# Performance work log

Hardware: AMD Instinct MI355X
Metric: run time of the kernel (lower is better)

The kernel has to match this reference:

```python
import jax, jax.numpy as jnp
import numpy as np

BS, N = 8, 2000
ALPHA = 0.2  # LeakyReLU slope
NEG = -9e15


def _gat_head(x, adj, W, a):
    # x: [bs,N,Fin], W: [Fin,Fout], a: [2*Fout]
    h = x @ W                                   # [bs,N,F]
    F_ = W.shape[-1]
    # e_ij = lrelu(h_i . a[:F] + h_j . a[F:])  (decomposed form of concat+matmul)
    src = h @ a[:F_]                            # [bs,N]
    dst = h @ a[F_:]                            # [bs,N]
    e = jax.nn.leaky_relu(src[:, :, None] + dst[:, None, :], ALPHA)  # [bs,N,N]
    att = jnp.where(adj[None] > 0, e, NEG)
    att = jax.nn.softmax(att, axis=-1)
    return jax.nn.elu(att @ h)                  # [bs,N,F]


def _gat_multihead(x, adj, W, a):
    # W: [H,Fin,Fout], a: [H,2*Fout] -> concat heads on feature dim
    out = jax.vmap(_gat_head, in_axes=(None, None, 0, 0))(x, adj, W, a)  # [H,bs,N,F]
    H, bs, n, F_ = out.shape
    return jnp.moveaxis(out, 0, 2).reshape(bs, n, H * F_)


def setup_inputs() -> dict:
    key = jax.random.key(0)
    ks = jax.random.split(key, 20)
    g = 1.414

    def xavu(k, shape, gain=1.0):
        fan_in, fan_out = shape[-2], shape[-1]
        lim = gain * np.sqrt(6.0 / (fan_in + fan_out))
        return jax.random.uniform(k, shape, jnp.float32, -lim, lim)

    x = jax.random.normal(ks[0], (BS, N, 1), jnp.float32)
    adj = jax.random.randint(ks[1], (N, N), 0, 2).astype(jnp.float32)
    inp = {
        "x": x, "adj": adj,
        "W1": xavu(ks[2], (4, 1, 8), g), "a1": xavu(ks[3], (4, 16, 1), g)[..., 0],
        "W2": xavu(ks[4], (3, 32, 16), g), "a2": xavu(ks[5], (3, 32, 1), g)[..., 0],
        "pw1": xavu(ks[6], (32, 1))[:, 0], "pb1": jnp.zeros((1,), jnp.float32),
        "pw2": xavu(ks[7], (48, 1))[:, 0], "pb2": jnp.zeros((1,), jnp.float32),
        "fc1_w": xavu(ks[8], (3 * N, 600)), "fc1_b": jnp.zeros((600,), jnp.float32),
        "fc2_w": xavu(ks[9], (600, 256)), "fc2_b": jnp.zeros((256,), jnp.float32),
        "fc3_w": xavu(ks[10], (256, 64)), "fc3_b": jnp.zeros((64,), jnp.float32),
        "fc4_w": xavu(ks[11], (64, 32)), "fc4_b": jnp.zeros((32,), jnp.float32),
        "fc5_w": xavu(ks[12], (32, 2)), "fc5_b": jnp.zeros((2,), jnp.float32),
    }
    return inp


def reference(x, adj, W1, a1, W2, a2, pw1, pb1, pw2, pb2,
              fc1_w, fc1_b, fc2_w, fc2_b, fc3_w, fc3_b, fc4_w, fc4_b, fc5_w, fc5_b):
    # dropout layers are identity in eval mode
    x0 = jnp.mean(x, axis=-1)                       # [bs,N]
    h = _gat_multihead(x, adj, W1, a1)              # [bs,N,32]
    x1 = h @ pw1 + pb1                              # [bs,N]
    h = _gat_multihead(h, adj, W2, a2)              # [bs,N,48]
    x2 = h @ pw2 + pb2                              # [bs,N]
    z = jnp.concatenate([x0, x1, x2], axis=1)       # [bs,3N]
    z = jax.nn.elu(z @ fc1_w + fc1_b)
    z = jax.nn.elu(z @ fc2_w + fc2_b)
    z1 = jax.nn.elu(z @ fc3_w + fc3_b)              # output [bs,64]
    z = jax.nn.elu(z1 @ fc4_w + fc4_b)
    gat_out = z @ fc5_w + fc5_b                     # [bs,2]
    return (z1, gat_out)
```

## Files before the change

kernel.cpp:

```cpp
#include <hip/hip_runtime.h>
#include <hip/hip_bf16.h>
#include <cmath>

#define N_NODES 2000
#define BS 8

typedef __attribute__((ext_vector_type(8))) short short8v;
typedef __attribute__((ext_vector_type(4))) float float4v;

__device__ __forceinline__ float elu_f(float v) { return v > 0.f ? v : expm1f(v); }

__device__ __forceinline__ unsigned short f32_bf16u(float f) {
    __hip_bfloat16 h = __float2bfloat16(f);
    unsigned short u;
    __builtin_memcpy(&u, &h, 2);
    return u;
}
__device__ __forceinline__ short f32_bf16(float f) { return (short)f32_bf16u(f); }

__device__ __forceinline__ unsigned cvt_pk_bf16(float a, float b) {
    unsigned r;
    asm("v_cvt_pk_bf16_f32 %0, %1, %2" : "=v"(r) : "v"(a), "v"(b));
    return r;
}

__global__ __launch_bounds__(256) void pack_kernel(
    const float* __restrict__ adj,
    unsigned* __restrict__ maskT32,
    short* __restrict__ hT) {
    int bx = blockIdx.x;
    int tid = threadIdx.x;
    if (bx < N_NODES) {
        int row = bx;
        int lane = tid & 63, wv = tid >> 6;
        for (int wq = wv; wq < 32; wq += 4) {
            int j = wq * 64 + lane;
            bool on = (j < N_NODES) && (adj[(size_t)row * N_NODES + j] > 0.f);
            unsigned long long bal = __ballot(on);
            if (lane == 0) {
                maskT32[(size_t)(2 * wq) * 2048 + row] = (unsigned)bal;
                maskT32[(size_t)(2 * wq + 1) * 2048 + row] = (unsigned)(bal >> 32);
            }
        }
        return;
    }
    for (int i = tid; i < 24 * 16 * 48; i += 256) {
        int bh = i / 768, rem = i % 768, f = rem / 48, n = N_NODES + rem % 48;
        hT[((size_t)bh * 16 + f) * 2048 + n] = 0;
    }
}

__global__ __launch_bounds__(256) void att1_kernel(
    const unsigned* __restrict__ maskT32,
    const float* __restrict__ x,
    const float* __restrict__ W1, const float* __restrict__ a1,
    float* __restrict__ o1) {
    __shared__ float2 sPQ[2048];
    __shared__ short sXb[2048];
    __shared__ float2 redmm[256];
    int tid = threadIdx.x;
    int head = blockIdx.y, b = blockIdx.z;

    float ws = 0.f, wd = 0.f;
    #pragma unroll
    for (int f = 0; f < 8; ++f) {
        float wv = W1[head * 8 + f];
        ws = fmaf(wv, a1[head * 16 + f], ws);
        wd = fmaf(wv, a1[head * 16 + 8 + f], wd);
    }

    float mn = 1e30f, mx = -1e30f;
    for (int n = tid; n < 2048; n += 256) {
        float xv = (n < N_NODES) ? x[(size_t)b * N_NODES + n] : 0.f;
        sXb[n] = f32_bf16(xv);
        if (n < N_NODES) { mn = fminf(mn, xv); mx = fmaxf(mx, xv); }
    }
    redmm[tid] = make_float2(mn, mx);
    __syncthreads();
    for (int s = 128; s > 0; s >>= 1) {
        if (tid < s) {
            redmm[tid].x = fminf(redmm[tid].x, redmm[tid + s].x);
            redmm[tid].y = fmaxf(redmm[tid].y, redmm[tid + s].y);
        }
        __syncthreads();
    }
    float md = wd >= 0.f ? wd * redmm[0].y : wd * redmm[0].x;

    for (int n = tid; n < 2048; n += 256) {
        if (n < N_NODES) {
            float d = wd * x[(size_t)b * N_NODES + n] - md;
            sPQ[n] = make_float2(__expf(d), __expf(0.2f * d));
        } else {
            sPQ[n] = make_float2(0.f, 0.f);
        }
    }
    __syncthreads();

    int lane = tid & 63;
    int wave = __builtin_amdgcn_readfirstlane(tid >> 6);
    int t = blockIdx.x * 4 + wave;
    if (t >= 125) return;
    int rs = lane & 15;
    int g = lane >> 4;
    int row = t * 16 + rs;

    float xr = x[(size_t)b * N_NODES + row];
    float u = ws * xr + md;
    float c = __expf(-0.8f * u);

    unsigned fill = (rs == 1) ? 0x3F803F80u : 0u;
    bool isx = (rs == 0);

    float4v acc = {0.f, 0.f, 0.f, 0.f};

    for (int jc = 0; jc < 64; ++jc) {
        int jb = jc * 32 + g * 8;
        float w[8];
        #pragma unroll
        for (int e2 = 0; e2 < 4; ++e2) {
            float4 pq2 = *(const float4*)(&sPQ[jb + e2 * 2]);
            w[e2 * 2 + 0] = fmaxf(pq2.x, c * pq2.y);
            w[e2 * 2 + 1] = fmaxf(pq2.z, c * pq2.w);
        }
        unsigned mby = maskT32[(size_t)jc * 2048 + row] >> (g * 8);
        #pragma unroll
        for (int e = 0; e < 8; ++e)
            w[e] = (mby & (1u << e)) ? w[e] : 0.f;
        uint4 au;
        au.x = cvt_pk_bf16(w[0], w[1]);
        au.y = cvt_pk_bf16(w[2], w[3]);
        au.z = cvt_pk_bf16(w[4], w[5]);
        au.w = cvt_pk_bf16(w[6], w[7]);
        short8v av;
        __builtin_memcpy(&av, &au, 16);
        uint4 xv4 = *(const uint4*)(sXb + jb);
        uint4 bu;
        bu.x = isx ? xv4.x : fill;
        bu.y = isx ? xv4.y : fill;
        bu.z = isx ? xv4.z : fill;
        bu.w = isx ? xv4.w : fill;
        short8v bv;
        __builtin_memcpy(&bv, &bu, 16);
        acc = __builtin_amdgcn_mfma_f32_16x16x32_bf16(av, bv, acc, 0, 0, 0);
    }

    #pragma unroll
    for (int reg = 0; reg < 4; ++reg) {
        int crow = g * 4 + reg;
        float nm = __shfl(acc[reg], lane & 48, 64);
        float dn = __shfl(acc[reg], (lane & 48) | 1, 64);
        float ratio = dn > 0.f ? nm / dn : 0.f;
        if (rs < 8) {
            float v = ratio * W1[head * 8 + rs];
            v = v > 0.f ? v : expm1f(v);
            o1[((size_t)(b * N_NODES + t * 16 + crow)) * 32 + head * 8 + rs] = v;
        }
    }
}

__global__ __launch_bounds__(256) void prep2_kernel(
    const float* __restrict__ o1, const float* __restrict__ W2,
    const float* __restrict__ a2,
    short* __restrict__ hT, float* __restrict__ s2, float* __restrict__ d2) {
    __shared__ float sW[1536];
    int tid = threadIdx.x;
    for (int i = tid; i < 1536; i += 256) sW[i] = W2[i];
    __syncthreads();
    int idx = blockIdx.x * 256 + tid;
    if (idx >= BS * 3 * N_NODES) return;
    int b = idx / 6000, r = idx % 6000, h = r / N_NODES, n = r % N_NODES;
    int bh = b * 3 + h;
    float in[32];
    const float4* ip = (const float4*)(o1 + ((size_t)b * N_NODES + n) * 32);
    #pragma unroll
    for (int q = 0; q < 8; ++q) {
        float4 v = ip[q];
        in[4 * q] = v.x; in[4 * q + 1] = v.y; in[4 * q + 2] = v.z; in[4 * q + 3] = v.w;
    }
    float hv[16];
    #pragma unroll
    for (int f = 0; f < 16; ++f) hv[f] = 0.f;
    #pragma unroll
    for (int k = 0; k < 32; ++k) {
        float ik = in[k];
        #pragma unroll
        for (int f = 0; f < 16; ++f) hv[f] = fmaf(ik, sW[h * 512 + k * 16 + f], hv[f]);
    }
    float sr = 0.f, ds = 0.f;
    #pragma unroll
    for (int f = 0; f < 16; ++f) {
        hT[((size_t)bh * 16 + f) * 2048 + n] = f32_bf16(hv[f]);
        sr = fmaf(hv[f], a2[h * 32 + f], sr);
        ds = fmaf(hv[f], a2[h * 32 + 16 + f], ds);
    }
    s2[(size_t)bh * N_NODES + n] = sr;
    d2[(size_t)bh * N_NODES + n] = ds;
}

__global__ __launch_bounds__(256) void att2_kernel(
    const unsigned* __restrict__ maskT32,
    const short* __restrict__ hT,
    const float* __restrict__ s2, const float* __restrict__ d2,
    float* __restrict__ o2) {
    __shared__ float2 sPQ[2048];
    __shared__ float red[256];
    int tid = threadIdx.x;
    int head = blockIdx.y, b = blockIdx.z, bh = b * 3 + head;
    const float* dp = d2 + (size_t)bh * N_NODES;

    float mx = -1e30f;
    for (int n = tid; n < N_NODES; n += 256) mx = fmaxf(mx, dp[n]);
    red[tid] = mx;
    __syncthreads();
    for (int s = 128; s > 0; s >>= 1) {
        if (tid < s) red[tid] = fmaxf(red[tid], red[tid + s]);
        __syncthreads();
    }
    float md = red[0];
    for (int n = tid; n < 2048; n += 256) {
        if (n < N_NODES) {
            float d = dp[n] - md;
            sPQ[n] = make_float2(__expf(d), __expf(0.2f * d));
        } else {
            sPQ[n] = make_float2(0.f, 0.f);
        }
    }
    __syncthreads();

    int lane = tid & 63;
    int wave = __builtin_amdgcn_readfirstlane(tid >> 6);
    int t = blockIdx.x * 4 + wave;
    if (t >= 125) return;
    int rs = lane & 15;
    int g = lane >> 4;
    int row = t * 16 + rs;

    float sv = s2[(size_t)bh * N_NODES + row];
    float u = sv + md;
    float c = __expf(-0.8f * u);
    const short* hb = hT + ((size_t)bh * 16 + rs) * 2048;

    const unsigned one2 = 0x3F803F80u;
    uint4 ou = make_uint4(one2, one2, one2, one2);
    short8v onesv;
    __builtin_memcpy(&onesv, &ou, 16);

    float4v acc = {0.f, 0.f, 0.f, 0.f};
    float4v accd = {0.f, 0.f, 0.f, 0.f};

    for (int jc = 0; jc < 64; ++jc) {
        int jb = jc * 32 + g * 8;
        float w[8];
        #pragma unroll
        for (int e2 = 0; e2 < 4; ++e2) {
            float4 pq2 = *(const float4*)(&sPQ[jb + e2 * 2]);
            w[e2 * 2 + 0] = fmaxf(pq2.x, c * pq2.y);
            w[e2 * 2 + 1] = fmaxf(pq2.z, c * pq2.w);
        }
        unsigned mby = maskT32[(size_t)jc * 2048 + row] >> (g * 8);
        #pragma unroll
        for (int e = 0; e < 8; ++e)
            w[e] = (mby & (1u << e)) ? w[e] : 0.f;
        uint4 au;
        au.x = cvt_pk_bf16(w[0], w[1]);
        au.y = cvt_pk_bf16(w[2], w[3]);
        au.z = cvt_pk_bf16(w[4], w[5]);
        au.w = cvt_pk_bf16(w[6], w[7]);
        short8v av;
        __builtin_memcpy(&av, &au, 16);
        short8v bv = *(const short8v*)(hb + jb);
        acc = __builtin_amdgcn_mfma_f32_16x16x32_bf16(av, bv, acc, 0, 0, 0);
        accd = __builtin_amdgcn_mfma_f32_16x16x32_bf16(av, onesv, accd, 0, 0, 0);
    }

    #pragma unroll
    for (int reg = 0; reg < 4; ++reg) {
        int crow = g * 4 + reg;
        float dn = accd[reg];
        float v = dn > 0.f ? acc[reg] / dn : 0.f;
        v = v > 0.f ? v : expm1f(v);
        o2[((size_t)(b * N_NODES + t * 16 + crow)) * 48 + head * 16 + rs] = v;
    }
}

__global__ __launch_bounds__(256) void fc1_splitk_kernel(
    const float* __restrict__ x,
    const float* __restrict__ o1, const float* __restrict__ o2,
    const float* __restrict__ pw1, const float* __restrict__ pb1,
    const float* __restrict__ pw2, const float* __restrict__ pb2,
    const float* __restrict__ W, float* __restrict__ partial) {
    const int K = 6000, O = 600, KS = 71;
    __shared__ float sz[BS][KS];
    int tid = threadIdx.x;
    int kt = blockIdx.y;
    int k0 = kt * KS;
    int len = (k0 + KS <= K) ? KS : (K - k0);
    float pb1v = pb1[0], pb2v = pb2[0];
    for (int i = tid; i < BS * len; i += 256) {
        int bb = i / len, k = k0 + i % len;
        float v;
        if (k < 2000) {
            v = x[bb * 2000 + k];
        } else if (k < 4000) {
            const float* op = o1 + ((size_t)bb * 2000 + (k - 2000)) * 32;
            float s = pb1v;
            #pragma unroll
            for (int q = 0; q < 32; ++q) s = fmaf(op[q], pw1[q], s);
            v = s;
        } else {
            const float* op = o2 + ((size_t)bb * 2000 + (k - 4000)) * 48;
            float s = pb2v;
            #pragma unroll
            for (int q = 0; q < 48; ++q) s = fmaf(op[q], pw2[q], s);
            v = s;
        }
        sz[bb][i % len] = v;
    }
    __syncthreads();
    int o = blockIdx.x * 256 + tid;
    float acc[BS] = {0.f, 0.f, 0.f, 0.f, 0.f, 0.f, 0.f, 0.f};
    if (o < O) {
        for (int k = 0; k < len; ++k) {
            float w = W[(size_t)(k0 + k) * O + o];
            #pragma unroll
            for (int b = 0; b < BS; ++b) acc[b] = fmaf(sz[b][k], w, acc[b]);
        }
        #pragma unroll
        for (int b = 0; b < BS; ++b)
            partial[((size_t)kt * BS + b) * O + o] = acc[b];
    }
}

__global__ __launch_bounds__(256) void fc2_splitk_kernel(
    const float* __restrict__ p1, const float* __restrict__ b1,
    const float* __restrict__ W, float* __restrict__ partial) {
    const int K = 600, O = 256, KS = 38;
    __shared__ float sz[BS][KS];
    int tid = threadIdx.x;
    int kt = blockIdx.y;
    int k0 = kt * KS;
    int k1 = k0 + KS < K ? k0 + KS : K;
    int len = k1 - k0;
    for (int i = tid; i < BS * len; i += 256) {
        int bb = i / len, k = k0 + i % len;
        float a = b1[k];
        #pragma unroll 5
        for (int q = 0; q < 85; ++q) a += p1[((size_t)q * BS + bb) * 600 + k];
        sz[bb][i % len] = elu_f(a);
    }
    __syncthreads();
    int o = tid;
    float acc[BS] = {0.f, 0.f, 0.f, 0.f, 0.f, 0.f, 0.f, 0.f};
    for (int k = 0; k < len; ++k) {
        float w = W[(size_t)(k0 + k) * O + o];
        #pragma unroll
        for (int b = 0; b < BS; ++b) acc[b] = fmaf(sz[b][k], w, acc[b]);
    }
    #pragma unroll
    for (int b = 0; b < BS; ++b)
        partial[((size_t)kt * BS + b) * O + o] = acc[b];
}

__global__ __launch_bounds__(256) void fc_tail_kernel(
    const float* __restrict__ p2, const float* __restrict__ b2,
    const float* __restrict__ w3, const float* __restrict__ b3,
    const float* __restrict__ w4, const float* __restrict__ b4,
    const float* __restrict__ w5, const float* __restrict__ b5,
    float* __restrict__ outp) {
    int b = blockIdx.x, tid = threadIdx.x;
    __shared__ float t2[256], red[256], z1[64], z4[32];
    {
        float a = b2[tid];
        #pragma unroll
        for (int kt = 0; kt < 16; ++kt) a += p2[((size_t)kt * BS + b) * 256 + tid];
        t2[tid] = elu_f(a);
    }
    __syncthreads();
    {
        int o = tid & 63, ks = tid >> 6;
        float a = 0.f;
        for (int k = ks; k < 256; k += 4) a = fmaf(t2[k], w3[k * 64 + o], a);
        red[tid] = a;
        __syncthreads();
        if (ks == 0) {
            float v = red[o] + red[64 + o] + red[128 + o] + red[192 + o] + b3[o];
            v = elu_f(v);
            z1[o] = v;
            outp[b * 64 + o] = v;
        }
    }
    __syncthreads();
    if (tid < 32) {
        float v = b4[tid];
        #pragma unroll
        for (int k = 0; k < 64; ++k) v = fmaf(z1[k], w4[k * 32 + tid], v);
        z4[tid] = elu_f(v);
    }
    __syncthreads();
    if (tid < 2) {
        float v = b5[tid];
        #pragma unroll
        for (int k = 0; k < 32; ++k) v = fmaf(z4[k], w5[k * 2 + tid], v);
        outp[BS * 64 + b * 2 + tid] = v;
    }
}

extern "C" void kernel_launch(void* const* d_in, const int* in_sizes, int n_in,
                              void* d_out, int out_size, void* d_ws, size_t ws_size,
                              hipStream_t stream) {
    const float* x    = (const float*)d_in[0];
    const float* adj  = (const float*)d_in[1];
    const float* W1   = (const float*)d_in[2];
    const float* a1   = (const float*)d_in[3];
    const float* W2   = (const float*)d_in[4];
    const float* a2   = (const float*)d_in[5];
    const float* pw1  = (const float*)d_in[6];
    const float* pb1  = (const float*)d_in[7];
    const float* pw2  = (const float*)d_in[8];
    const float* pb2  = (const float*)d_in[9];
    const float* fc1w = (const float*)d_in[10];
    const float* fc1b = (const float*)d_in[11];
    const float* fc2w = (const float*)d_in[12];
    const float* fc2b = (const float*)d_in[13];
    const float* fc3w = (const float*)d_in[14];
    const float* fc3b = (const float*)d_in[15];
    const float* fc4w = (const float*)d_in[16];
    const float* fc4b = (const float*)d_in[17];
    const float* fc5w = (const float*)d_in[18];
    const float* fc5b = (const float*)d_in[19];
    float* outp = (float*)d_out;

    float* ws = (float*)d_ws;
    size_t off = 0;
    auto alloc = [&](size_t n) {
        float* p = ws + off;
        off += (n + 63) & ~(size_t)63;
        return p;
    };
    float* o1 = alloc((size_t)BS * N_NODES * 32);
    float* s2 = alloc((size_t)24 * N_NODES);
    float* d2 = alloc((size_t)24 * N_NODES);
    short* hT = (short*)alloc((size_t)24 * 16 * 2048 / 2);
    float* o2 = alloc((size_t)BS * N_NODES * 48);
    const int KT1 = 85;
    float* p1 = alloc((size_t)KT1 * BS * 600);
    float* p2 = alloc((size_t)16 * BS * 256);
    unsigned* maskT32 = (unsigned*)alloc((size_t)64 * 2048);

    pack_kernel<<<N_NODES + 1, 256, 0, stream>>>(adj, maskT32, hT);
    att1_kernel<<<dim3(32, 4, BS), 256, 0, stream>>>(maskT32, x, W1, a1, o1);
    prep2_kernel<<<(BS * 3 * N_NODES + 255) / 256, 256, 0, stream>>>(o1, W2, a2, hT, s2, d2);
    att2_kernel<<<dim3(32, 3, BS), 256, 0, stream>>>(maskT32, hT, s2, d2, o2);
    fc1_splitk_kernel<<<dim3(3, KT1), 256, 0, stream>>>(
        x, o1, o2, pw1, pb1, pw2, pb2, fc1w, p1);
    fc2_splitk_kernel<<<dim3(1, 16), 256, 0, stream>>>(p1, fc1b, fc2w, p2);
    fc_tail_kernel<<<BS, 256, 0, stream>>>(
        p2, fc2b, fc3w, fc3b, fc4w, fc4b, fc5w, fc5b, outp);
}
```

Baseline: 130.3 us.

## Split attention neighbor dimension in halves with flash-style partial merge kernels

Both attention kernels now split the neighbor (j) dimension into two halves, doubling the grid. Each half computes its own max shift and writes unnormalized numerator and denominator partials, which new finish kernels rescale and merge before applying ELU. The x-to-bf16 conversion moves into pack_kernel, and the block reductions switch to wave shuffles. The aim is more parallelism and a shorter per-block serial loop, at the cost of two extra launches and extra global traffic for the partials.

```diff
diff --git a/kernel.cpp b/kernel.cpp
--- a/kernel.cpp
+++ b/kernel.cpp
@@ -18,16 +18,16 @@
 }
 __device__ __forceinline__ short f32_bf16(float f) { return (short)f32_bf16u(f); }
 
-__device__ __forceinline__ unsigned cvt_pk_bf16(float a, float b) {
+__device__ __forceinline__ unsigned cvt_pk_bf16(float lo, float hi) {
     unsigned r;
-    asm("v_cvt_pk_bf16_f32 %0, %1, %2" : "=v"(r) : "v"(a), "v"(b));
+    asm("v_cvt_pk_bf16_f32 %0, %1, %2" : "=v"(r) : "v"(lo), "v"(hi));
     return r;
 }
 
 __global__ __launch_bounds__(256) void pack_kernel(
-    const float* __restrict__ adj,
-    unsigned* __restrict__ maskT32,
-    short* __restrict__ hT) {
+    const float* __restrict__ adj, const float* __restrict__ x,
+    unsigned* __restrict__ maskT32, short* __restrict__ hT,
+    short* __restrict__ xb16) {
     int bx = blockIdx.x;
     int tid = threadIdx.x;
     if (bx < N_NODES) {
@@ -44,22 +44,31 @@
         }
         return;
     }
-    for (int i = tid; i < 24 * 16 * 48; i += 256) {
-        int bh = i / 768, rem = i % 768, f = rem / 48, n = N_NODES + rem % 48;
-        hT[((size_t)bh * 16 + f) * 2048 + n] = 0;
+    if (bx == N_NODES) {
+        for (int i = tid; i < 24 * 16 * 48; i += 256) {
+            int bh = i / 768, rem = i % 768, f = rem / 48, n = N_NODES + rem % 48;
+            hT[((size_t)bh * 16 + f) * 2048 + n] = 0;
+        }
+        return;
+    }
+    for (int i = tid; i < BS * 2048; i += 256) {
+        int b = i >> 11, n = i & 2047;
+        xb16[i] = (n < N_NODES) ? f32_bf16(x[(size_t)b * N_NODES + n]) : 0;
     }
 }
 
 __global__ __launch_bounds__(256) void att1_kernel(
     const unsigned* __restrict__ maskT32,
-    const float* __restrict__ x,
+    const float* __restrict__ x, const short* __restrict__ xb16,
     const float* __restrict__ W1, const float* __restrict__ a1,
-    float* __restrict__ o1) {
-    __shared__ float2 sPQ[2048];
-    __shared__ short sXb[2048];
-    __shared__ float2 redmm[256];
+    float* __restrict__ pn1, float* __restrict__ pd1, float* __restrict__ pmd1) {
+    __shared__ float2 sPQ[1024];
+    __shared__ float2 redmm[4];
     int tid = threadIdx.x;
-    int head = blockIdx.y, b = blockIdx.z;
+    int head = blockIdx.y;
+    int half = blockIdx.z & 1, b = blockIdx.z >> 1;
+    int bh = b * 4 + head;
+    int j0g = half * 1024;
 
     float ws = 0.f, wd = 0.f;
     #pragma unroll
@@ -70,28 +79,32 @@
     }
 
     float mn = 1e30f, mx = -1e30f;
-    for (int n = tid; n < 2048; n += 256) {
-        float xv = (n < N_NODES) ? x[(size_t)b * N_NODES + n] : 0.f;
-        sXb[n] = f32_bf16(xv);
-        if (n < N_NODES) { mn = fminf(mn, xv); mx = fmaxf(mx, xv); }
-    }
-    redmm[tid] = make_float2(mn, mx);
-    __syncthreads();
-    for (int s = 128; s > 0; s >>= 1) {
-        if (tid < s) {
-            redmm[tid].x = fminf(redmm[tid].x, redmm[tid + s].x);
-            redmm[tid].y = fmaxf(redmm[tid].y, redmm[tid + s].y);
-        }
-        __syncthreads();
-    }
-    float md = wd >= 0.f ? wd * redmm[0].y : wd * redmm[0].x;
-
-    for (int n = tid; n < 2048; n += 256) {
-        if (n < N_NODES) {
-            float d = wd * x[(size_t)b * N_NODES + n] - md;
-            sPQ[n] = make_float2(__expf(d), __expf(0.2f * d));
+    for (int i = tid; i < 1024; i += 256) {
+        int j = j0g + i;
+        if (j < N_NODES) {
+            float v = x[(size_t)b * N_NODES + j];
+            mn = fminf(mn, v); mx = fmaxf(mx, v);
+        }
+    }
+    #pragma unroll
+    for (int off = 32; off >= 1; off >>= 1) {
+        mn = fminf(mn, __shfl_xor(mn, off, 64));
+        mx = fmaxf(mx, __shfl_xor(mx, off, 64));
+    }
+    if ((tid & 63) == 0) redmm[tid >> 6] = make_float2(mn, mx);
+    __syncthreads();
+    mn = fminf(fminf(redmm[0].x, redmm[1].x), fminf(redmm[2].x, redmm[3].x));
+    mx = fmaxf(fmaxf(redmm[0].y, redmm[1].y), fmaxf(redmm[2].y, redmm[3].y));
+    float md = wd >= 0.f ? wd * mx : wd * mn;
+    if (tid == 0 && blockIdx.x == 0) pmd1[half * 32 + bh] = md;
+
+    for (int i = tid; i < 1024; i += 256) {
+        int j = j0g + i;
+        if (j < N_NODES) {
+            float d = wd * x[(size_t)b * N_NODES + j] - md;
+            sPQ[i] = make_float2(__expf(d), __expf(0.2f * d));
         } else {
-            sPQ[n] = make_float2(0.f, 0.f);
+            sPQ[i] = make_float2(0.f, 0.f);
         }
     }
     __syncthreads();
@@ -110,19 +123,22 @@
 
     unsigned fill = (rs == 1) ? 0x3F803F80u : 0u;
     bool isx = (rs == 0);
+    const short* xbp = xb16 + (size_t)b * 2048 + j0g;
 
     float4v acc = {0.f, 0.f, 0.f, 0.f};
 
-    for (int jc = 0; jc < 64; ++jc) {
-        int jb = jc * 32 + g * 8;
+    for (int jcl = 0; jcl < 32; ++jcl) {
+        int jb = jcl * 32 + g * 8;
+        float4 pqa0 = *(const float4*)(&sPQ[jb]);
+        float4 pqa1 = *(const float4*)(&sPQ[jb + 2]);
+        float4 pqa2 = *(const float4*)(&sPQ[jb + 4]);
+        float4 pqa3 = *(const float4*)(&sPQ[jb + 6]);
         float w[8];
-        #pragma unroll
-        for (int e2 = 0; e2 < 4; ++e2) {
-            float4 pq2 = *(const float4*)(&sPQ[jb + e2 * 2]);
-            w[e2 * 2 + 0] = fmaxf(pq2.x, c * pq2.y);
-            w[e2 * 2 + 1] = fmaxf(pq2.z, c * pq2.w);
-        }
-        unsigned mby = maskT32[(size_t)jc * 2048 + row] >> (g * 8);
+        w[0] = fmaxf(pqa0.x, c * pqa0.y); w[1] = fmaxf(pqa0.z, c * pqa0.w);
+        w[2] = fmaxf(pqa1.x, c * pqa1.y); w[3] = fmaxf(pqa1.z, c * pqa1.w);
+        w[4] = fmaxf(pqa2.x, c * pqa2.y); w[5] = fmaxf(pqa2.z, c * pqa2.w);
+        w[6] = fmaxf(pqa3.x, c * pqa3.y); w[7] = fmaxf(pqa3.z, c * pqa3.w);
+        unsigned mby = maskT32[(size_t)(half * 32 + jcl) * 2048 + row] >> (g * 8);
         #pragma unroll
         for (int e = 0; e < 8; ++e)
             w[e] = (mby & (1u << e)) ? w[e] : 0.f;
@@ -133,12 +149,9 @@
         au.w = cvt_pk_bf16(w[6], w[7]);
         short8v av;
         __builtin_memcpy(&av, &au, 16);
-        uint4 xv4 = *(const uint4*)(sXb + jb);
         uint4 bu;
-        bu.x = isx ? xv4.x : fill;
-        bu.y = isx ? xv4.y : fill;
-        bu.z = isx ? xv4.z : fill;
-        bu.w = isx ? xv4.w : fill;
+        if (isx) bu = *(const uint4*)(xbp + jb);
+        else bu = make_uint4(fill, fill, fill, fill);
         short8v bv;
         __builtin_memcpy(&bv, &bu, 16);
         acc = __builtin_amdgcn_mfma_f32_16x16x32_bf16(av, bv, acc, 0, 0, 0);
@@ -146,14 +159,34 @@
 
     #pragma unroll
     for (int reg = 0; reg < 4; ++reg) {
-        int crow = g * 4 + reg;
-        float nm = __shfl(acc[reg], lane & 48, 64);
-        float dn = __shfl(acc[reg], (lane & 48) | 1, 64);
-        float ratio = dn > 0.f ? nm / dn : 0.f;
-        if (rs < 8) {
-            float v = ratio * W1[head * 8 + rs];
-            v = v > 0.f ? v : expm1f(v);
-            o1[((size_t)(b * N_NODES + t * 16 + crow)) * 32 + head * 8 + rs] = v;
+        int crow = t * 16 + g * 4 + reg;
+        if (rs == 0) pn1[(size_t)(half * 32 + bh) * N_NODES + crow] = acc[reg];
+        if (rs == 1) pd1[(size_t)(half * 32 + bh) * N_NODES + crow] = acc[reg];
+    }
+}
+
+__global__ __launch_bounds__(256) void finish1_kernel(
+    const float* __restrict__ pn1, const float* __restrict__ pd1,
+    const float* __restrict__ pmd1, const float* __restrict__ W1,
+    float* __restrict__ o1) {
+    int idx = blockIdx.x * 256 + threadIdx.x;
+    if (idx >= BS * N_NODES) return;
+    int b = idx / N_NODES, n = idx % N_NODES;
+    #pragma unroll
+    for (int head = 0; head < 4; ++head) {
+        int bh = b * 4 + head;
+        float mdA = pmd1[bh], mdB = pmd1[32 + bh];
+        float U = fmaxf(mdA, mdB);
+        float sA = __expf(mdA - U), sB = __expf(mdB - U);
+        float num = pn1[(size_t)bh * N_NODES + n] * sA
+                  + pn1[(size_t)(32 + bh) * N_NODES + n] * sB;
+        float den = pd1[(size_t)bh * N_NODES + n] * sA
+                  + pd1[(size_t)(32 + bh) * N_NODES + n] * sB;
+        float ratio = den > 0.f ? num / den : 0.f;
+        #pragma unroll
+        for (int f = 0; f < 8; ++f) {
+            float v = ratio * W1[head * 8 + f];
+            o1[(size_t)idx * 32 + head * 8 + f] = v > 0.f ? v : expm1f(v);
         }
     }
 }
@@ -201,28 +234,36 @@
     const unsigned* __restrict__ maskT32,
     const short* __restrict__ hT,
     const float* __restrict__ s2, const float* __restrict__ d2,
-    float* __restrict__ o2) {
-    __shared__ float2 sPQ[2048];
-    __shared__ float red[256];
+    float* __restrict__ pn2, float* __restrict__ pd2, float* __restrict__ pmd2) {
+    __shared__ float2 sPQ[1024];
+    __shared__ float red[4];
     int tid = threadIdx.x;
-    int head = blockIdx.y, b = blockIdx.z, bh = b * 3 + head;
+    int head = blockIdx.y;
+    int half = blockIdx.z & 1, b = blockIdx.z >> 1;
+    int bh = b * 3 + head;
+    int j0g = half * 1024;
     const float* dp = d2 + (size_t)bh * N_NODES;
 
     float mx = -1e30f;
-    for (int n = tid; n < N_NODES; n += 256) mx = fmaxf(mx, dp[n]);
-    red[tid] = mx;
-    __syncthreads();
-    for (int s = 128; s > 0; s >>= 1) {
-        if (tid < s) red[tid] = fmaxf(red[tid], red[tid + s]);
-        __syncthreads();
-    }
-    float md = red[0];
-    for (int n = tid; n < 2048; n += 256) {
-        if (n < N_NODES) {
-            float d = dp[n] - md;
-            sPQ[n] = make_float2(__expf(d), __expf(0.2f * d));
+    for (int i = tid; i < 1024; i += 256) {
+        int j = j0g + i;
+        if (j < N_NODES) mx = fmaxf(mx, dp[j]);
+    }
+    #pragma unroll
+    for (int off = 32; off >= 1; off >>= 1)
+        mx = fmaxf(mx, __shfl_xor(mx, off, 64));
+    if ((tid & 63) == 0) red[tid >> 6] = mx;
+    __syncthreads();
+    float md = fmaxf(fmaxf(red[0], red[1]), fmaxf(red[2], red[3]));
+    if (tid == 0 && blockIdx.x == 0) pmd2[half * 24 + bh] = md;
+
+    for (int i = tid; i < 1024; i += 256) {
+        int j = j0g + i;
+        if (j < N_NODES) {
+            float d = dp[j] - md;
+            sPQ[i] = make_float2(__expf(d), __expf(0.2f * d));
         } else {
-            sPQ[n] = make_float2(0.f, 0.f);
+            sPQ[i] = make_float2(0.f, 0.f);
         }
     }
     __syncthreads();
@@ -238,7 +279,7 @@
     float sv = s2[(size_t)bh * N_NODES + row];
     float u = sv + md;
     float c = __expf(-0.8f * u);
-    const short* hb = hT + ((size_t)bh * 16 + rs) * 2048;
+    const short* hb = hT + ((size_t)bh * 16 + rs) * 2048 + j0g;
 
     const unsigned one2 = 0x3F803F80u;
     uint4 ou = make_uint4(one2, one2, one2, one2);
@@ -248,16 +289,18 @@
     float4v acc = {0.f, 0.f, 0.f, 0.f};
     float4v accd = {0.f, 0.f, 0.f, 0.f};
 
-    for (int jc = 0; jc < 64; ++jc) {
-        int jb = jc * 32 + g * 8;
+    for (int jcl = 0; jcl < 32; ++jcl) {
+        int jb = jcl * 32 + g * 8;
+        float4 pqa0 = *(const float4*)(&sPQ[jb]);
+        float4 pqa1 = *(const float4*)(&sPQ[jb + 2]);
+        float4 pqa2 = *(const float4*)(&sPQ[jb + 4]);
+        float4 pqa3 = *(const float4*)(&sPQ[jb + 6]);
         float w[8];
-        #pragma unroll
-        for (int e2 = 0; e2 < 4; ++e2) {
-            float4 pq2 = *(const float4*)(&sPQ[jb + e2 * 2]);
-            w[e2 * 2 + 0] = fmaxf(pq2.x, c * pq2.y);
-            w[e2 * 2 + 1] = fmaxf(pq2.z, c * pq2.w);
-        }
-        unsigned mby = maskT32[(size_t)jc * 2048 + row] >> (g * 8);
+        w[0] = fmaxf(pqa0.x, c * pqa0.y); w[1] = fmaxf(pqa0.z, c * pqa0.w);
+        w[2] = fmaxf(pqa1.x, c * pqa1.y); w[3] = fmaxf(pqa1.z, c * pqa1.w);
+        w[4] = fmaxf(pqa2.x, c * pqa2.y); w[5] = fmaxf(pqa2.z, c * pqa2.w);
+        w[6] = fmaxf(pqa3.x, c * pqa3.y); w[7] = fmaxf(pqa3.z, c * pqa3.w);
+        unsigned mby = maskT32[(size_t)(half * 32 + jcl) * 2048 + row] >> (g * 8);
         #pragma unroll
         for (int e = 0; e < 8; ++e)
             w[e] = (mby & (1u << e)) ? w[e] : 0.f;
@@ -275,11 +318,40 @@
 
     #pragma unroll
     for (int reg = 0; reg < 4; ++reg) {
-        int crow = g * 4 + reg;
-        float dn = accd[reg];
-        float v = dn > 0.f ? acc[reg] / dn : 0.f;
-        v = v > 0.f ? v : expm1f(v);
-        o2[((size_t)(b * N_NODES + t * 16 + crow)) * 48 + head * 16 + rs] = v;
+        int crow = t * 16 + g * 4 + reg;
+        pn2[((size_t)(half * 24 + bh) * N_NODES + crow) * 16 + rs] = acc[reg];
+        if (rs == 0) pd2[(size_t)(half * 24 + bh) * N_NODES + crow] = accd[reg];
+    }
+}
+
+__global__ __launch_bounds__(256) void finish2_kernel(
+    const float* __restrict__ pn2, const float* __restrict__ pd2,
+    const float* __restrict__ pmd2,
+    float* __restrict__ o2) {
+    int idx = blockIdx.x * 256 + threadIdx.x;
+    if (idx >= 24 * N_NODES) return;
+    int bh = idx / N_NODES, n = idx % N_NODES;
+    int b = bh / 3, h = bh % 3;
+    float mdA = pmd2[bh], mdB = pmd2[24 + bh];
+    float U = fmaxf(mdA, mdB);
+    float sA = __expf(mdA - U), sB = __expf(mdB - U);
+    float den = pd2[(size_t)bh * N_NODES + n] * sA
+              + pd2[(size_t)(24 + bh) * N_NODES + n] * sB;
+    float inv = den > 0.f ? 1.0f / den : 0.f;
+    const float4* pa = (const float4*)(pn2 + ((size_t)bh * N_NODES + n) * 16);
+    const float4* pb = (const float4*)(pn2 + ((size_t)(24 + bh) * N_NODES + n) * 16);
+    float* op = o2 + ((size_t)b * N_NODES + n) * 48 + h * 16;
+    #pragma unroll
+    for (int q = 0; q < 4; ++q) {
+        float4 va = pa[q], vb = pb[q];
+        float v0 = (va.x * sA + vb.x * sB) * inv;
+        float v1 = (va.y * sA + vb.y * sB) * inv;
+        float v2 = (va.z * sA + vb.z * sB) * inv;
+        float v3 = (va.w * sA + vb.w * sB) * inv;
+        op[4 * q + 0] = v0 > 0.f ? v0 : expm1f(v0);
+        op[4 * q + 1] = v1 > 0.f ? v1 : expm1f(v1);
+        op[4 * q + 2] = v2 > 0.f ? v2 : expm1f(v2);
+        op[4 * q + 3] = v3 > 0.f ? v3 : expm1f(v3);
     }
 }
 
@@ -437,20 +509,32 @@
         off += (n + 63) & ~(size_t)63;
         return p;
     };
-    float* o1 = alloc((size_t)BS * N_NODES * 32);
-    float* s2 = alloc((size_t)24 * N_NODES);
-    float* d2 = alloc((size_t)24 * N_NODES);
-    short* hT = (short*)alloc((size_t)24 * 16 * 2048 / 2);
-    float* o2 = alloc((size_t)BS * N_NODES * 48);
+    float* o1  = alloc((size_t)BS * N_NODES * 32);
+    float* s2  = alloc((size_t)24 * N_NODES);
+    float* d2  = alloc((size_t)24 * N_NODES);
+    short* hT  = (short*)alloc((size_t)24 * 16 * 2048 / 2);
+    short* xb16 = (short*)alloc((size_t)BS * 2048 / 2);
+    float* o2  = alloc((size_t)BS * N_NODES * 48);
     const int KT1 = 85;
-    float* p1 = alloc((size_t)KT1 * BS * 600);
-    float* p2 = alloc((size_t)16 * BS * 256);
+    float* p1  = alloc((size_t)KT1 * BS * 600);
+    float* p2  = alloc((size_t)16 * BS * 256);
+    float* pn1 = alloc((size_t)2 * 32 * N_NODES);
+    float* pd1 = alloc((size_t)2 * 32 * N_NODES);
+    float* pmd1 = alloc(64);
+    float* pn2 = alloc((size_t)2 * 24 * N_NODES * 16);
+    float* pd2 = alloc((size_t)2 * 24 * N_NODES);
+    float* pmd2 = alloc(64);
     unsigned* maskT32 = (unsigned*)alloc((size_t)64 * 2048);
 
-    pack_kernel<<<N_NODES + 1, 256, 0, stream>>>(adj, maskT32, hT);
-    att1_kernel<<<dim3(32, 4, BS), 256, 0, stream>>>(maskT32, x, W1, a1, o1);
+    pack_kernel<<<N_NODES + 2, 256, 0, stream>>>(adj, x, maskT32, hT, xb16);
+    att1_kernel<<<dim3(32, 4, BS * 2), 256, 0, stream>>>(
+        maskT32, x, xb16, W1, a1, pn1, pd1, pmd1);
+    finish1_kernel<<<(BS * N_NODES + 255) / 256, 256, 0, stream>>>(
+        pn1, pd1, pmd1, W1, o1);
     prep2_kernel<<<(BS * 3 * N_NODES + 255) / 256, 256, 0, stream>>>(o1, W2, a2, hT, s2, d2);
-    att2_kernel<<<dim3(32, 3, BS), 256, 0, stream>>>(maskT32, hT, s2, d2, o2);
+    att2_kernel<<<dim3(32, 3, BS * 2), 256, 0, stream>>>(
+        maskT32, hT, s2, d2, pn2, pd2, pmd2);
+    finish2_kernel<<<(24 * N_NODES + 255) / 256, 256, 0, stream>>>(pn2, pd2, pmd2, o2);
     fc1_splitk_kernel<<<dim3(3, KT1), 256, 0, stream>>>(
         x, o1, o2, pw1, pb1, pw2, pb2, fc1w, p1);
     fc2_splitk_kernel<<<dim3(1, 16), 256, 0, stream>>>(p1, fc1b, fc2w, p2);
```

Result: slower. 157.7 us (+21.0%).
